# Performance work log

Measured on AMD Instinct MI355X. Metric: run time of the kernel, lower is better.

The kernel has to match this reference:

```python
import jax, jax.numpy as jnp
import numpy as np

D = 1024   # n_embd
H = 16     # n_head
HD = D // H

def setup_inputs() -> dict:
    key = jax.random.key(0)
    ks = jax.random.split(key, 6)
    s = 1.0 / np.sqrt(D)
    x  = jax.random.normal(ks[0], (4, 2048, D), dtype=jnp.float32)
    Wq = jax.random.uniform(ks[1], (D, D), jnp.float32, -s, s)
    Wk = jax.random.uniform(ks[2], (D, D), jnp.float32, -s, s)
    Wv = jax.random.uniform(ks[3], (D, D), jnp.float32, -s, s)
    Wp = jax.random.uniform(ks[4], (D, D), jnp.float32, -s, s)
    bp = jax.random.uniform(ks[5], (D,),   jnp.float32, -s, s)
    return {"x": x, "Wq": Wq, "Wk": Wk, "Wv": Wv, "Wp": Wp, "bp": bp}

def reference(x, Wq, Wk, Wv, Wp, bp):
    B, T, C = x.shape
    scale = 1.0 / np.sqrt(HD)
    # torch nn.Linear: y = x @ W.T
    q = (x @ Wq.T).reshape(B, T, H, HD).transpose(0, 2, 1, 3)  # [B,H,T,hd]
    k = (x @ Wk.T).reshape(B, T, H, HD).transpose(0, 2, 1, 3)
    v = (x @ Wv.T).reshape(B, T, H, HD).transpose(0, 2, 1, 3)
    att = jnp.einsum('bhqd,bhkd->bhqk', q, k) * scale           # [B,H,T,T]
    causal = jnp.tril(jnp.ones((T, T), dtype=bool))
    att = jnp.where(causal[None, None], att, -jnp.inf)
    att = jax.nn.softmax(att, axis=-1)
    y = jnp.einsum('bhqk,bhkd->bhqd', att, v)                   # [B,H,T,hd]
    y = y.transpose(0, 2, 1, 3).reshape(B, T, C)
    return y @ Wp.T + bp
```

## Files before the change

### kernel.cpp

```cpp
#include <hip/hip_runtime.h>
#include <hip/hip_bf16.h>
#include <math.h>


#define B_  4
#define T_  2048
#define D_  1024
#define H_  16
#define HD_ 64
#define M_  (B_ * T_)

typedef short bf16x8 __attribute__((ext_vector_type(8)));
typedef float f32x4  __attribute__((ext_vector_type(4)));

__device__ __forceinline__ f32x4 mfma16(bf16x8 a, bf16x8 b, f32x4 c) {
    return __builtin_amdgcn_mfma_f32_16x16x32_bf16(a, b, c, 0, 0, 0);
}

__device__ __forceinline__ void gl_lds16(const unsigned short* g, unsigned short* l) {
    __builtin_amdgcn_global_load_lds(
        (const __attribute__((address_space(1))) void*)g,
        (__attribute__((address_space(3))) void*)l, 16, 0, 0);
}

__device__ __forceinline__ unsigned short f2bf(float f) {
    union { __hip_bfloat16 h; unsigned short u; } cv;
    cv.h = __float2bfloat16(f);
    return cv.u;
}
__device__ __forceinline__ float bf2f(unsigned short u) {
    return __uint_as_float(((unsigned)u) << 16);
}
__device__ __forceinline__ float exp2_fast(float x) {
    return __builtin_amdgcn_exp2f(x);
}

struct su4 { unsigned short x, y, z, w; };

__global__ __launch_bounds__(256)
void cvt_kernel(const float* __restrict__ in, unsigned short* __restrict__ out) {
    const int i = blockIdx.x * 256 + threadIdx.x;
    const float4 v = ((const float4*)in)[i];
    su4 o;
    o.x = f2bf(v.x); o.y = f2bf(v.y); o.z = f2bf(v.z); o.w = f2bf(v.w);
    ((su4*)out)[i] = o;
}

__global__ __launch_bounds__(256)
void cvtw_kernel(const float* __restrict__ w0, const float* __restrict__ w1,
                 const float* __restrict__ w2, const float* __restrict__ w3,
                 unsigned short* __restrict__ o0, unsigned short* __restrict__ o1,
                 unsigned short* __restrict__ o2, unsigned short* __restrict__ o3) {
    const int y = blockIdx.y;
    const float* in       = (y == 0) ? w0 : (y == 1) ? w1 : (y == 2) ? w2 : w3;
    unsigned short* out   = (y == 0) ? o0 : (y == 1) ? o1 : (y == 2) ? o2 : o3;
    const int i = blockIdx.x * 256 + threadIdx.x;
    const float4 v = ((const float4*)in)[i];
    su4 o;
    o.x = f2bf(v.x); o.y = f2bf(v.y); o.z = f2bf(v.z); o.w = f2bf(v.w);
    ((su4*)out)[i] = o;
}

__global__ __launch_bounds__(256, 2)
void qkv_kernel(const unsigned short* __restrict__ X,
                const unsigned short* __restrict__ Wq,
                const unsigned short* __restrict__ Wk,
                const unsigned short* __restrict__ Wv,
                unsigned short* __restrict__ Qo,
                unsigned short* __restrict__ Ko,
                unsigned short* __restrict__ Vo)
{
    __shared__ unsigned short As[128 * 64];
    __shared__ unsigned short Bs[128 * 64];

    const int m0 = blockIdx.x * 128;
    const int by = blockIdx.y;
    const unsigned short* W = (by < 8) ? Wq : (by < 16) ? Wk : Wv;
    unsigned short*       O = (by < 8) ? Qo : (by < 16) ? Ko : Vo;
    const int n0   = (by & 7) * 128;
    const bool vsec = (by >= 16);
    const int tid  = threadIdx.x;
    const int lane = tid & 63;
    const int wv   = tid >> 6;
    const int wr   = (wv >> 1) * 64;
    const int wc   = (wv & 1) * 64;
    const int g    = lane >> 4;
    const int c    = lane & 15;

    f32x4 acc[4][4] = {};

    for (int k0 = 0; k0 < D_; k0 += 64) {
        #pragma unroll
        for (int i = 0; i < 4; ++i) {
            const int flat = i * 2048 + tid * 8;
            const int row = flat >> 6, col = flat & 63;
            gl_lds16(X + (size_t)(m0 + row) * D_ + k0 + col, As + flat);
            gl_lds16(W + (size_t)(n0 + row) * D_ + k0 + col, Bs + flat);
        }
        __syncthreads();
        #pragma unroll
        for (int kk = 0; kk < 64; kk += 32) {
            bf16x8 af[4], bg[4];
            #pragma unroll
            for (int mi = 0; mi < 4; ++mi)
                af[mi] = *(const bf16x8*)(As + (wr + mi * 16 + c) * 64 + kk + g * 8);
            #pragma unroll
            for (int ni = 0; ni < 4; ++ni)
                bg[ni] = *(const bf16x8*)(Bs + (wc + ni * 16 + c) * 64 + kk + g * 8);
            if (!vsec) {
                #pragma unroll
                for (int mi = 0; mi < 4; ++mi)
                    #pragma unroll
                    for (int ni = 0; ni < 4; ++ni)
                        acc[mi][ni] = mfma16(af[mi], bg[ni], acc[mi][ni]);
            } else {
                #pragma unroll
                for (int mi = 0; mi < 4; ++mi)
                    #pragma unroll
                    for (int ni = 0; ni < 4; ++ni)
                        acc[mi][ni] = mfma16(bg[ni], af[mi], acc[mi][ni]);
            }
        }
        __syncthreads();
    }

    if (!vsec) {
        #pragma unroll
        for (int mi = 0; mi < 4; ++mi)
            #pragma unroll
            for (int ni = 0; ni < 4; ++ni)
                #pragma unroll
                for (int r = 0; r < 4; ++r) {
                    const int m = m0 + wr + mi * 16 + g * 4 + r;
                    const int n = n0 + wc + ni * 16 + c;
                    const int b = m >> 11, t = m & (T_ - 1);
                    const int h = n >> 6,  hd = n & 63;
                    O[((size_t)((b << 4) + h) * T_ + t) * HD_ + hd] = f2bf(acc[mi][ni][r]);
                }
    } else {
        #pragma unroll
        for (int mi = 0; mi < 4; ++mi)
            #pragma unroll
            for (int ni = 0; ni < 4; ++ni)
                #pragma unroll
                for (int r = 0; r < 4; ++r) {
                    const int n = n0 + wc + ni * 16 + g * 4 + r;
                    const int m = m0 + wr + mi * 16 + c;
                    const int b = m >> 11, t = m & (T_ - 1);
                    const int h = n >> 6,  hd = n & 63;
                    O[((size_t)((b << 4) + h) * HD_ + hd) * T_ + t] = f2bf(acc[mi][ni][r]);
                }
    }
}

__device__ __forceinline__ bf16x8 ptrans(const f32x4& p0, const f32x4& p1,
                                         int lane, int g, int c) {
    unsigned int P32[2][2];
    P32[0][0] = (unsigned int)f2bf(p0[0]) | ((unsigned int)f2bf(p0[1]) << 16);
    P32[0][1] = (unsigned int)f2bf(p0[2]) | ((unsigned int)f2bf(p0[3]) << 16);
    P32[1][0] = (unsigned int)f2bf(p1[0]) | ((unsigned int)f2bf(p1[1]) << 16);
    P32[1][1] = (unsigned int)f2bf(p1[2]) | ((unsigned int)f2bf(p1[3]) << 16);
    const int sl0 = c + ((lane & 16) << 1);
    const int sl1 = sl0 + 16;
    const int q00 = __shfl((int)P32[0][0], sl0), q10 = __shfl((int)P32[1][0], sl0);
    const int q01 = __shfl((int)P32[0][1], sl0), q11 = __shfl((int)P32[1][1], sl0);
    const int q02 = __shfl((int)P32[0][0], sl1), q12 = __shfl((int)P32[1][0], sl1);
    const int q03 = __shfl((int)P32[0][1], sl1), q13 = __shfl((int)P32[1][1], sl1);
    const bool nhi = (g & 2) != 0;
    union { unsigned int u[4]; bf16x8 v; } pf;
    pf.u[0] = nhi ? q10 : q00;
    pf.u[1] = nhi ? q11 : q01;
    pf.u[2] = nhi ? q12 : q02;
    pf.u[3] = nhi ? q13 : q03;
    return pf.v;
}

__global__ __launch_bounds__(256, 4)
void attn_kernel(const unsigned short* __restrict__ Q,
                 const unsigned short* __restrict__ K,
                 const unsigned short* __restrict__ VT,
                 unsigned short* __restrict__ Y)
{
    __shared__ unsigned short Ks[4096];
    __shared__ unsigned short Vs[4096];

    const int bh = blockIdx.x;
    const int qt = 31 - blockIdx.y;
    const unsigned short* Qp  = Q  + (size_t)bh * T_ * HD_;
    const unsigned short* Kp  = K  + (size_t)bh * T_ * HD_;
    const unsigned short* VTp = VT + (size_t)bh * HD_ * T_;
    const int b = bh >> 4, h = bh & 15;

    const int tid  = threadIdx.x;
    const int lane = tid & 63;
    const int w    = tid >> 6;
    const int g    = lane >> 4;
    const int c    = lane & 15;
    const float SC = 0.18033688011112042f;

    const int qw = qt * 64 + w * 16;
    const int nt = qt + 1;

    int srow[2], scol[2];
    #pragma unroll
    for (int i = 0; i < 2; ++i) {
        const int L = (i * 256 + tid) * 16;
        srow[i] = L >> 7;
        scol[i] = (L & 127) ^ ((srow[i] & 3) << 5);
    }

    bf16x8 qf[2];
    #pragma unroll
    for (int dk = 0; dk < 2; ++dk) {
        bf16x8 t = *(const bf16x8*)(Qp + (size_t)(qw + c) * HD_ + dk * 32 + g * 8);
        #pragma unroll
        for (int j = 0; j < 8; ++j)
            t[j] = (short)f2bf(bf2f((unsigned short)t[j]) * SC);
        qf[dk] = t;
    }

    float m_l = -1e30f, l_l = 0.f;
    f32x4 oacc[4] = {};

    for (int ti = 0; ti < nt; ++ti) {
        const int tb = ti << 6;
        const bool last = (ti == nt - 1);

        #pragma unroll
        for (int i = 0; i < 2; ++i) {
            const int L = (i * 256 + tid) * 16;
            gl_lds16(Kp + (size_t)(tb + srow[i]) * HD_ + (scol[i] >> 1),
                     Ks + (L >> 1));
            gl_lds16(VTp + (size_t)srow[i] * T_ + tb + (scol[i] >> 1),
                     Vs + (L >> 1));
        }
        __syncthreads();

        f32x4 sA[2] = {}, sB[2] = {};
        #pragma unroll
        for (int ni = 0; ni < 2; ++ni)
            #pragma unroll
            for (int dk = 0; dk < 2; ++dk) {
                const int rA = ni * 16 + c;
                const int rB = 32 + ni * 16 + c;
                const bf16x8 kA = *(const bf16x8*)((const char*)Ks
                    + rA * 128 + ((dk * 64 + g * 16) ^ ((c & 3) << 5)));
                const bf16x8 kB = *(const bf16x8*)((const char*)Ks
                    + rB * 128 + ((dk * 64 + g * 16) ^ ((c & 3) << 5)));
                sA[ni] = mfma16(kA, qf[dk], sA[ni]);
                sB[ni] = mfma16(kB, qf[dk], sB[ni]);
            }

        if (last) {
            #pragma unroll
            for (int ni = 0; ni < 2; ++ni)
                #pragma unroll
                for (int r = 0; r < 4; ++r) {
                    const int kA = tb + ni * 16 + g * 4 + r;
                    sA[ni][r] = (kA      <= qw + c) ? sA[ni][r] : -1e30f;
                    sB[ni][r] = (kA + 32 <= qw + c) ? sB[ni][r] : -1e30f;
                }
        }

        float pmax = sA[0][0];
        #pragma unroll
        for (int ni = 0; ni < 2; ++ni)
            #pragma unroll
            for (int r = 0; r < 4; ++r) {
                pmax = fmaxf(pmax, sA[ni][r]);
                pmax = fmaxf(pmax, sB[ni][r]);
            }
        pmax = fmaxf(pmax, __shfl_xor(pmax, 16));
        pmax = fmaxf(pmax, __shfl_xor(pmax, 32));

        const bool skip = __all(pmax - m_l <= 8.0f);
        float al = 1.f;
        if (!skip) {
            const float mn = fmaxf(m_l, pmax);
            al = exp2_fast(m_l - mn);
            m_l = mn;
        }

        float rs = 0.f;
        #pragma unroll
        for (int ni = 0; ni < 2; ++ni)
            #pragma unroll
            for (int r = 0; r < 4; ++r) {
                const float eA = exp2_fast(sA[ni][r] - m_l);
                const float eB = exp2_fast(sB[ni][r] - m_l);
                sA[ni][r] = eA; sB[ni][r] = eB;
                rs += eA + eB;
            }
        rs += __shfl_xor(rs, 16);
        rs += __shfl_xor(rs, 32);
        l_l = l_l * al + rs;

        const bf16x8 pfA = ptrans(sA[0], sA[1], lane, g, c);
        const bf16x8 pfB = ptrans(sB[0], sB[1], lane, g, c);

        #pragma unroll
        for (int dn = 0; dn < 4; ++dn) {
            const int row = dn * 16 + c;
            const bf16x8 vA = *(const bf16x8*)((const char*)Vs
                + row * 128 + ((g * 16)      ^ ((c & 3) << 5)));
            const bf16x8 vB = *(const bf16x8*)((const char*)Vs
                + row * 128 + ((64 + g * 16) ^ ((c & 3) << 5)));
            if (!skip) {
                #pragma unroll
                for (int r = 0; r < 4; ++r)
                    oacc[dn][r] *= al;
            }
            oacc[dn] = mfma16(vA, pfA, oacc[dn]);
            oacc[dn] = mfma16(vB, pfB, oacc[dn]);
        }
        __syncthreads();
    }

    const float li = 1.f / l_l;
    const size_t rowoff = (size_t)(b * T_ + qw + c) * D_ + h * 64;
    #pragma unroll
    for (int dn = 0; dn < 4; ++dn) {
        const unsigned int u0 = (unsigned int)f2bf(oacc[dn][0] * li)
                              | ((unsigned int)f2bf(oacc[dn][1] * li) << 16);
        const unsigned int u1 = (unsigned int)f2bf(oacc[dn][2] * li)
                              | ((unsigned int)f2bf(oacc[dn][3] * li) << 16);
        uint2 st; st.x = u0; st.y = u1;
        *(uint2*)(Y + rowoff + dn * 16 + g * 4) = st;
    }
}

__global__ __launch_bounds__(256, 2)
void proj_kernel(const unsigned short* __restrict__ Yin,
                 const unsigned short* __restrict__ Wp,
                 const float* __restrict__ bp,
                 float* __restrict__ Out)
{
    __shared__ unsigned short As[128 * 64];
    __shared__ unsigned short Bs[128 * 64];

    const int m0 = blockIdx.x * 128;
    const int n0 = blockIdx.y * 128;
    const int tid  = threadIdx.x;
    const int lane = tid & 63;
    const int wv   = tid >> 6;
    const int wr   = (wv >> 1) * 64;
    const int wc   = (wv & 1) * 64;
    const int g    = lane >> 4;
    const int c    = lane & 15;

    f32x4 acc[4][4] = {};

    for (int k0 = 0; k0 < D_; k0 += 64) {
        #pragma unroll
        for (int i = 0; i < 4; ++i) {
            const int flat = i * 2048 + tid * 8;
            const int row = flat >> 6, col = flat & 63;
            gl_lds16(Yin + (size_t)(m0 + row) * D_ + k0 + col, As + flat);
            gl_lds16(Wp  + (size_t)(n0 + row) * D_ + k0 + col, Bs + flat);
        }
        __syncthreads();
        #pragma unroll
        for (int kk = 0; kk < 64; kk += 32) {
            bf16x8 af[4], bg[4];
            #pragma unroll
            for (int mi = 0; mi < 4; ++mi)
                af[mi] = *(const bf16x8*)(As + (wr + mi * 16 + c) * 64 + kk + g * 8);
            #pragma unroll
            for (int ni = 0; ni < 4; ++ni)
                bg[ni] = *(const bf16x8*)(Bs + (wc + ni * 16 + c) * 64 + kk + g * 8);
            #pragma unroll
            for (int mi = 0; mi < 4; ++mi)
                #pragma unroll
                for (int ni = 0; ni < 4; ++ni)
                    acc[mi][ni] = mfma16(af[mi], bg[ni], acc[mi][ni]);
        }
        __syncthreads();
    }

    #pragma unroll
    for (int mi = 0; mi < 4; ++mi) {
        #pragma unroll
        for (int ni = 0; ni < 4; ++ni) {
            const int n = n0 + wc + ni * 16 + c;
            const float bb = bp[n];
            #pragma unroll
            for (int r = 0; r < 4; ++r) {
                const int m = m0 + wr + mi * 16 + g * 4 + r;
                Out[(size_t)m * D_ + n] = acc[mi][ni][r] + bb;
            }
        }
    }
}

extern "C" void kernel_launch(void* const* d_in, const int* in_sizes, int n_in,
                              void* d_out, int out_size, void* d_ws, size_t ws_size,
                              hipStream_t stream) {
    const float* x  = (const float*)d_in[0];
    const float* Wq = (const float*)d_in[1];
    const float* Wk = (const float*)d_in[2];
    const float* Wv = (const float*)d_in[3];
    const float* Wp = (const float*)d_in[4];
    const float* bp = (const float*)d_in[5];
    float* out = (float*)d_out;

    const size_t SZ  = (size_t)M_ * D_;
    const size_t WSZ = (size_t)D_ * D_;
    unsigned short* ws = (unsigned short*)d_ws;
    unsigned short* XB  = ws;
    unsigned short* WQB = XB  + SZ;
    unsigned short* WKB = WQB + WSZ;
    unsigned short* WVB = WKB + WSZ;
    unsigned short* WPB = WVB + WSZ;
    unsigned short* Qw  = WPB + WSZ;
    unsigned short* Kw  = Qw + SZ;
    unsigned short* Vw  = Kw + SZ;
    unsigned short* Yw  = XB;

    dim3 blk(256);
    cvt_kernel <<<dim3(SZ / 1024),     blk, 0, stream>>>(x, XB);
    cvtw_kernel<<<dim3(WSZ / 1024, 4), blk, 0, stream>>>(Wq, Wk, Wv, Wp, WQB, WKB, WVB, WPB);

    qkv_kernel <<<dim3(M_ / 128, 24), blk, 0, stream>>>(XB, WQB, WKB, WVB, Qw, Kw, Vw);
    attn_kernel<<<dim3(B_ * H_, T_ / 64), blk, 0, stream>>>(Qw, Kw, Vw, Yw);
    proj_kernel<<<dim3(M_ / 128, D_ / 128), blk, 0, stream>>>(Yw, WPB, bp, out);
}
```

Before: 205.4 us.

## Double-buffer K/V tiles in attention kernel with prefetch of next tile

K and V shared-memory tiles become two-slot buffers. The next tile's global-to-LDS loads are issued before computing on the current tile, so load latency overlaps the QK, softmax and PV work, and one barrier per iteration is removed. Wave priority is raised around the MFMA section. This doubles LDS use per block, which could limit occupancy under the 4-blocks launch bound.

```diff
diff --git a/kernel.cpp b/kernel.cpp
--- a/kernel.cpp
+++ b/kernel.cpp
@@ -181,8 +181,8 @@
                  const unsigned short* __restrict__ VT,
                  unsigned short* __restrict__ Y)
 {
-    __shared__ unsigned short Ks[4096];
-    __shared__ unsigned short Vs[4096];
+    __shared__ unsigned short Ks[2][4096];
+    __shared__ unsigned short Vs[2][4096];
 
     const int bh = blockIdx.x;
     const int qt = 31 - blockIdx.y;
@@ -221,32 +221,41 @@
 
     float m_l = -1e30f, l_l = 0.f;
     f32x4 oacc[4] = {};
+    const int swz = (c & 3) << 5;
+
+    auto stage = [&](int buf, int tb) {
+        #pragma unroll
+        for (int i = 0; i < 2; ++i) {
+            const int L = (i * 256 + tid) * 16;
+            gl_lds16(Kp + (size_t)(tb + srow[i]) * HD_ + (scol[i] >> 1),
+                     &Ks[buf][L >> 1]);
+            gl_lds16(VTp + (size_t)srow[i] * T_ + tb + (scol[i] >> 1),
+                     &Vs[buf][L >> 1]);
+        }
+    };
+
+    stage(0, 0);
+    __syncthreads();
+    int cur = 0;
 
     for (int ti = 0; ti < nt; ++ti) {
         const int tb = ti << 6;
         const bool last = (ti == nt - 1);
 
-        #pragma unroll
-        for (int i = 0; i < 2; ++i) {
-            const int L = (i * 256 + tid) * 16;
-            gl_lds16(Kp + (size_t)(tb + srow[i]) * HD_ + (scol[i] >> 1),
-                     Ks + (L >> 1));
-            gl_lds16(VTp + (size_t)srow[i] * T_ + tb + (scol[i] >> 1),
-                     Vs + (L >> 1));
-        }
-        __syncthreads();
-
+        if (!last) stage(cur ^ 1, tb + 64);
+
+        __builtin_amdgcn_s_setprio(1);
+
+        const char* Kb = (const char*)Ks[cur];
+        const char* Vb = (const char*)Vs[cur];
         f32x4 sA[2] = {}, sB[2] = {};
         #pragma unroll
         for (int ni = 0; ni < 2; ++ni)
             #pragma unroll
             for (int dk = 0; dk < 2; ++dk) {
-                const int rA = ni * 16 + c;
-                const int rB = 32 + ni * 16 + c;
-                const bf16x8 kA = *(const bf16x8*)((const char*)Ks
-                    + rA * 128 + ((dk * 64 + g * 16) ^ ((c & 3) << 5)));
-                const bf16x8 kB = *(const bf16x8*)((const char*)Ks
-                    + rB * 128 + ((dk * 64 + g * 16) ^ ((c & 3) << 5)));
+                const int col = (dk * 64 + g * 16) ^ swz;
+                const bf16x8 kA = *(const bf16x8*)(Kb + (ni * 16 + c) * 128 + col);
+                const bf16x8 kB = *(const bf16x8*)(Kb + (32 + ni * 16 + c) * 128 + col);
                 sA[ni] = mfma16(kA, qf[dk], sA[ni]);
                 sB[ni] = mfma16(kB, qf[dk], sB[ni]);
             }
@@ -301,10 +310,8 @@
         #pragma unroll
         for (int dn = 0; dn < 4; ++dn) {
             const int row = dn * 16 + c;
-            const bf16x8 vA = *(const bf16x8*)((const char*)Vs
-                + row * 128 + ((g * 16)      ^ ((c & 3) << 5)));
-            const bf16x8 vB = *(const bf16x8*)((const char*)Vs
-                + row * 128 + ((64 + g * 16) ^ ((c & 3) << 5)));
+            const bf16x8 vA = *(const bf16x8*)(Vb + row * 128 + ((g * 16)      ^ swz));
+            const bf16x8 vB = *(const bf16x8*)(Vb + row * 128 + ((64 + g * 16) ^ swz));
             if (!skip) {
                 #pragma unroll
                 for (int r = 0; r < 4; ++r)
@@ -313,7 +320,10 @@
             oacc[dn] = mfma16(vA, pfA, oacc[dn]);
             oacc[dn] = mfma16(vB, pfB, oacc[dn]);
         }
+
+        __builtin_amdgcn_s_setprio(0);
         __syncthreads();
+        cur ^= 1;
     }
 
     const float li = 1.f / l_l;
```

Result: no change. 202.7 us (-1.3%).
